# Kernel optimization log

Hardware: AMD Instinct MI355X
Metric: run time of the kernel (lower is better)

The kernel has to match this reference:

```python
import jax, jax.numpy as jnp
import numpy as np

HEADS = 16
DIM_HEAD = 64
QUERY_DIM = 1024
INNER_DIM = HEADS * DIM_HEAD  # 1024
SCALE = DIM_HEAD ** -0.5


def setup_inputs() -> dict:
    key = jax.random.key(0)
    ks = jax.random.split(key, 6)
    B, S = 2, 2048
    hidden_states = jax.random.normal(ks[0], (B, S, QUERY_DIM), dtype=jnp.float32)
    # torch Linear weights are [out, in]; store transposed [in, out] for x @ W
    w_q = jax.random.normal(ks[1], (QUERY_DIM, INNER_DIM), dtype=jnp.float32) * (QUERY_DIM ** -0.5)
    w_k = jax.random.normal(ks[2], (QUERY_DIM, INNER_DIM), dtype=jnp.float32) * (QUERY_DIM ** -0.5)
    w_v = jax.random.normal(ks[3], (QUERY_DIM, INNER_DIM), dtype=jnp.float32) * (QUERY_DIM ** -0.5)
    w_o = jax.random.normal(ks[4], (INNER_DIM, QUERY_DIM), dtype=jnp.float32) * (INNER_DIM ** -0.5)
    b_o = jax.random.normal(ks[5], (QUERY_DIM,), dtype=jnp.float32) * 0.01
    return {"hidden_states": hidden_states, "w_q": w_q, "w_k": w_k, "w_v": w_v, "w_o": w_o, "b_o": b_o}


def reference(hidden_states, w_q, w_k, w_v, w_o, b_o):
    B, S, _ = hidden_states.shape
    # QKV projections (context = hidden_states, i.e. self-attention)
    q = (hidden_states @ w_q).reshape(B, S, HEADS, DIM_HEAD)
    k = (hidden_states @ w_k).reshape(B, S, HEADS, DIM_HEAD)
    v = (hidden_states @ w_v).reshape(B, S, HEADS, DIM_HEAD)
    # scaled dot-product attention; scores materialized as [B, H, S, S]
    scores = jnp.einsum("bqhd,bkhd->bhqk", q, k) * SCALE
    probs = jax.nn.softmax(scores, axis=-1)
    out = jnp.einsum("bhqk,bkhd->bqhd", probs, v).reshape(B, S, INNER_DIM)
    return out @ w_o + b_o
```

## Files before the change

kernel.cpp:

```cpp
#include <hip/hip_runtime.h>
#include <cstdint>
#include <cstddef>

typedef unsigned short u16;
typedef unsigned int u32;
typedef __bf16 bf16x8 __attribute__((ext_vector_type(8)));
typedef float f32x4 __attribute__((ext_vector_type(4)));
typedef float f32x16 __attribute__((ext_vector_type(16)));
typedef u32 u32x2 __attribute__((ext_vector_type(2)));
typedef u32 u32x4 __attribute__((ext_vector_type(4)));

#define AS1 __attribute__((address_space(1)))
#define AS3 __attribute__((address_space(3)))

__device__ __forceinline__ void gld16(const u16* g, u16* l) {
  __builtin_amdgcn_global_load_lds((const AS1 void*)(const void*)g,
                                   (AS3 void*)(void*)l, 16, 0, 0);
}

__device__ __forceinline__ u16 f2bf(float f) {
  union { float f; unsigned u; } x; x.f = f;
  return (u16)((x.u + 0x7fffu + ((x.u >> 16) & 1u)) >> 16);
}

__device__ __forceinline__ float bf2f(u16 u) {
  union { u32 i; float f; } x; x.i = ((u32)u) << 16; return x.f;
}

__device__ __forceinline__ f32x16 zf16() {
  f32x16 v;
#pragma unroll
  for (int i = 0; i < 16; ++i) v[i] = 0.f;
  return v;
}

__global__ void k_cvt(const float* __restrict__ in, u16* __restrict__ out, int n4) {
  int i = blockIdx.x * blockDim.x + threadIdx.x;
  if (i >= n4) return;
  float4 v = reinterpret_cast<const float4*>(in)[i];
  ushort4 o;
  o.x = f2bf(v.x); o.y = f2bf(v.y); o.z = f2bf(v.z); o.w = f2bf(v.w);
  reinterpret_cast<ushort4*>(out)[i] = o;
}

__global__ void k_tr4(const float* __restrict__ wq, const float* __restrict__ wk,
                      const float* __restrict__ wv, const float* __restrict__ wo,
                      u16* __restrict__ Wqkv, u16* __restrict__ Wot) {
  __shared__ float t[32][33];
  const int z = blockIdx.z;
  const float* in = (z == 0) ? wq : (z == 1) ? wk : (z == 2) ? wv : wo;
  u16* out = (z < 3) ? (Wqkv + (size_t)z * 1048576) : Wot;
  int bx = blockIdx.x * 32, by = blockIdx.y * 32;
  int tx = threadIdx.x, ty = threadIdx.y;
#pragma unroll
  for (int j = 0; j < 32; j += 8)
    t[ty + j][tx] = in[(size_t)(by + ty + j) * 1024 + bx + tx];
  __syncthreads();
#pragma unroll
  for (int j = 0; j < 32; j += 8)
    out[(size_t)(bx + ty + j) * 1024 + by + tx] = f2bf(t[tx][ty + j]);
}

__global__ __launch_bounds__(256) void k_gemm_qkv(
    const u16* __restrict__ Xb,
    const u16* __restrict__ Wt,
    u16* __restrict__ Qb,
    u16* __restrict__ Kb,
    u16* __restrict__ Vt) {
  __shared__ __align__(16) u16 As[128][32];
  __shared__ __align__(16) u16 Bs[128][32];
  const int tid = threadIdx.x;
  const int w = tid >> 6, l = tid & 63;
  const int bm = blockIdx.x * 128;
  const int bn = blockIdx.y * 128;
  const int wm = (w >> 1) * 64, wn = (w & 1) * 64;
  const int lm = l & 15, lg = l >> 4;

  f32x4 acc[4][4];
#pragma unroll
  for (int i = 0; i < 4; ++i)
#pragma unroll
    for (int j = 0; j < 4; ++j) acc[i][j] = f32x4{0.f, 0.f, 0.f, 0.f};

  const int srow = w * 16 + (l >> 2);
  const int scol = (l & 3) * 8;
  for (int k0 = 0; k0 < 1024; k0 += 32) {
#pragma unroll
    for (int j = 0; j < 2; ++j) {
      gld16(Xb + (size_t)(bm + j * 64 + srow) * 1024 + k0 + scol, &As[j * 64 + w * 16][0]);
      gld16(Wt + (size_t)(bn + j * 64 + srow) * 1024 + k0 + scol, &Bs[j * 64 + w * 16][0]);
    }
    __syncthreads();
    bf16x8 af[4], bfr[4];
#pragma unroll
    for (int mt = 0; mt < 4; ++mt)
      af[mt] = *reinterpret_cast<const bf16x8*>(&As[wm + mt * 16 + lm][lg * 8]);
#pragma unroll
    for (int nt = 0; nt < 4; ++nt)
      bfr[nt] = *reinterpret_cast<const bf16x8*>(&Bs[wn + nt * 16 + lm][lg * 8]);
#pragma unroll
    for (int mt = 0; mt < 4; ++mt)
#pragma unroll
      for (int nt = 0; nt < 4; ++nt)
        acc[mt][nt] = __builtin_amdgcn_mfma_f32_16x16x32_bf16(af[mt], bfr[nt], acc[mt][nt], 0, 0, 0);
    __syncthreads();
  }
#pragma unroll
  for (int nt = 0; nt < 4; ++nt) {
    int gc = bn + wn + nt * 16 + lm;
    int which = gc >> 10, jc = gc & 1023, h = jc >> 6, d = jc & 63;
#pragma unroll
    for (int mt = 0; mt < 4; ++mt) {
#pragma unroll
      for (int r = 0; r < 4; ++r) {
        int gr = bm + wm + mt * 16 + lg * 4 + r;
        int b = gr >> 11, s = gr & 2047;
        float v = acc[mt][nt][r];
        size_t bh = (size_t)(b * 16 + h);
        if (which == 0)      Qb[(bh * 2048 + s) * 64 + d] = f2bf(v * 0.18033688f);
        else if (which == 1) Kb[(bh * 2048 + s) * 64 + d] = f2bf(v);
        else                 Vt[(bh * 64 + d) * 2048 + s] = f2bf(v);
      }
    }
  }
}

__global__ __launch_bounds__(256) void k_attn(
    const u16* __restrict__ Qb, const u16* __restrict__ Kb,
    const u16* __restrict__ Vt, u16* __restrict__ Opb,
    float* __restrict__ ml) {
  __shared__ __align__(16) u16 Ks[2][64][64];
  __shared__ __align__(16) u16 Vs[2][64][64];
  __shared__ float scb[4][32];
  const int tid = threadIdx.x, w = tid >> 6, l = tid & 63;
  const int lm = l & 31, hi = l >> 5;
  const int kx = lm & 7;
  const int bh = blockIdx.x;
  const int q0 = blockIdx.y * 128 + w * 32;
  const int z = blockIdx.z;
  const int kvbase = z * 1024;
  const u16* Qh = Qb + (size_t)bh * 2048 * 64;
  const u16* Kh = Kb + ((size_t)bh * 2048 + kvbase) * 64;
  const u16* Vh = Vt + (size_t)bh * 64 * 2048 + kvbase;

  bf16x8 qf[4];
#pragma unroll
  for (int c = 0; c < 4; ++c)
    qf[c] = *reinterpret_cast<const bf16x8*>(&Qh[(size_t)(q0 + lm) * 64 + 16 * c + 8 * hi]);

  f32x16 oacc0 = zf16(), oacc1 = zf16();
  float m = -1e30f, lsum = 0.f;

  const int r4 = l >> 2;
  const int vrow = w * 16 + r4;

  {
    u32x2 vreg[2][2];
#pragma unroll
    for (int ch = 0; ch < 2; ++ch) {
      int pg = ((l & 3) + 4 * (r4 & 1) + 4 * ch) & 7;
      int g = pg ^ (r4 & 7);
      int base = ((g >> 1) << 4) | ((g & 1) << 2);
      const u16* src = Vh + (size_t)vrow * 2048 + base;
      vreg[ch][0] = *reinterpret_cast<const u32x2*>(src);
      vreg[ch][1] = *reinterpret_cast<const u32x2*>(src + 8);
    }
#pragma unroll
    for (int j = 0; j < 2; ++j) {
      int row = w * 16 + j * 8 + (l >> 3);
      int g = (l & 7) ^ (row & 7);
      gld16(Kh + (size_t)row * 64 + 8 * g, &Ks[0][w * 16 + j * 8][0]);
    }
#pragma unroll
    for (int ch = 0; ch < 2; ++ch) {
      int pg = ((l & 3) + 4 * (r4 & 1) + 4 * ch) & 7;
      u32x4 pk;
      pk[0] = vreg[ch][0][0]; pk[1] = vreg[ch][0][1];
      pk[2] = vreg[ch][1][0]; pk[3] = vreg[ch][1][1];
      *reinterpret_cast<u32x4*>(&Vs[0][vrow][pg * 8]) = pk;
    }
  }
  __syncthreads();

  for (int t = 0; t < 16; ++t) {
    const int cur = t & 1, nxt = cur ^ 1;
    const int kvn = (t + 1) * 64;
    u32x2 vreg[2][2];
    if (t < 15) {
#pragma unroll
      for (int ch = 0; ch < 2; ++ch) {
        int pg = ((l & 3) + 4 * (r4 & 1) + 4 * ch) & 7;
        int g = pg ^ (r4 & 7);
        int base = ((g >> 1) << 4) | ((g & 1) << 2);
        const u16* src = Vh + (size_t)vrow * 2048 + kvn + base;
        vreg[ch][0] = *reinterpret_cast<const u32x2*>(src);
        vreg[ch][1] = *reinterpret_cast<const u32x2*>(src + 8);
      }
#pragma unroll
      for (int j = 0; j < 2; ++j) {
        int row = w * 16 + j * 8 + (l >> 3);
        int g = (l & 7) ^ (row & 7);
        gld16(Kh + (size_t)(kvn + row) * 64 + 8 * g, &Ks[nxt][w * 16 + j * 8][0]);
      }
    }

    const u16* Kc = &Ks[cur][0][0];
    f32x16 st0 = zf16(), st1 = zf16();
#pragma unroll
    for (int c = 0; c < 4; ++c) {
      bf16x8 kf0 = *reinterpret_cast<const bf16x8*>(Kc + (size_t)lm * 64 + 8 * ((2 * c + hi) ^ kx));
      st0 = __builtin_amdgcn_mfma_f32_32x32x16_bf16(kf0, qf[c], st0, 0, 0, 0);
    }
#pragma unroll
    for (int c = 0; c < 4; ++c) {
      bf16x8 kf1 = *reinterpret_cast<const bf16x8*>(Kc + (size_t)(32 + lm) * 64 + 8 * ((2 * c + hi) ^ kx));
      st1 = __builtin_amdgcn_mfma_f32_32x32x16_bf16(kf1, qf[c], st1, 0, 0, 0);
    }

    float tm = st0[0];
#pragma unroll
    for (int r = 1; r < 16; ++r) tm = fmaxf(tm, st0[r]);
#pragma unroll
    for (int r = 0; r < 16; ++r) tm = fmaxf(tm, st1[r]);
    tm = fmaxf(tm, __shfl_xor(tm, 32));
    if (!__all(tm - m <= 8.0f)) {
      float mnew = fmaxf(m, tm);
      scb[w][lm] = exp2f(m - mnew);
      asm volatile("s_waitcnt lgkmcnt(0)" ::: "memory");
      __builtin_amdgcn_sched_barrier(0);
      lsum *= exp2f(m - mnew);
#pragma unroll
      for (int r = 0; r < 16; ++r) {
        int cr = (r & 3) + 8 * (r >> 2) + 4 * hi;
        float s = scb[w][cr];
        oacc0[r] *= s; oacc1[r] *= s;
      }
      m = mnew;
    }
    float ps = 0.f;
    bf16x8 pf[2][2];
#pragma unroll
    for (int j = 0; j < 2; ++j)
#pragma unroll
      for (int ii = 0; ii < 8; ++ii) {
        float p0 = exp2f(st0[8 * j + ii] - m);
        float p1 = exp2f(st1[8 * j + ii] - m);
        ps += p0 + p1;
        pf[0][j][ii] = (__bf16)p0;
        pf[1][j][ii] = (__bf16)p1;
      }
    ps += __shfl_xor(ps, 32);
    lsum += ps;

    const u16* Vc = &Vs[cur][0][0];
#pragma unroll
    for (int tt = 0; tt < 2; ++tt)
#pragma unroll
      for (int j = 0; j < 2; ++j) {
        int gA = (4 * tt + 2 * j + hi) ^ kx;
        bf16x8 v0 = *reinterpret_cast<const bf16x8*>(Vc + (size_t)lm * 64 + 8 * gA);
        bf16x8 v1 = *reinterpret_cast<const bf16x8*>(Vc + (size_t)(32 + lm) * 64 + 8 * gA);
        oacc0 = __builtin_amdgcn_mfma_f32_32x32x16_bf16(pf[tt][j], v0, oacc0, 0, 0, 0);
        oacc1 = __builtin_amdgcn_mfma_f32_32x32x16_bf16(pf[tt][j], v1, oacc1, 0, 0, 0);
      }

    if (t < 15) {
#pragma unroll
      for (int ch = 0; ch < 2; ++ch) {
        int pg = ((l & 3) + 4 * (r4 & 1) + 4 * ch) & 7;
        u32x4 pk;
        pk[0] = vreg[ch][0][0]; pk[1] = vreg[ch][0][1];
        pk[2] = vreg[ch][1][0]; pk[3] = vreg[ch][1][1];
        *reinterpret_cast<u32x4*>(&Vs[nxt][vrow][pg * 8]) = pk;
      }
    }
    __syncthreads();
  }

  const size_t zb = (size_t)(z * 32 + bh);
  if (!hi) {
    float2 v; v.x = m; v.y = lsum;
    *reinterpret_cast<float2*>(&ml[(zb * 2048 + q0 + lm) * 2]) = v;
  }
  const size_t robase = zb * 2048 + q0;
#pragma unroll
  for (int r = 0; r < 16; ++r) {
    int cr = (r & 3) + 8 * (r >> 2) + 4 * hi;
    size_t ro = (robase + cr) * 64;
    Opb[ro + lm]      = f2bf(oacc0[r]);
    Opb[ro + 32 + lm] = f2bf(oacc1[r]);
  }
}

__global__ __launch_bounds__(256) void k_merge(
    const u16* __restrict__ Opb, const float* __restrict__ ml,
    u16* __restrict__ Ab) {
  int idx = blockIdx.x * 256 + threadIdx.x;
  int d8 = idx & 7, q = (idx >> 3) & 2047, bh = idx >> 14;
  size_t r0 = (size_t)bh * 2048 + q;
  size_t r1 = (size_t)(32 + bh) * 2048 + q;
  float2 ml0 = *reinterpret_cast<const float2*>(&ml[r0 * 2]);
  float2 ml1 = *reinterpret_cast<const float2*>(&ml[r1 * 2]);
  float M = fmaxf(ml0.x, ml1.x);
  float w0 = exp2f(ml0.x - M), w1 = exp2f(ml1.x - M);
  float inv = 1.0f / (w0 * ml0.y + w1 * ml1.y);
  w0 *= inv; w1 *= inv;
  u32x4 a0 = *reinterpret_cast<const u32x4*>(&Opb[r0 * 64 + d8 * 8]);
  u32x4 a1 = *reinterpret_cast<const u32x4*>(&Opb[r1 * 64 + d8 * 8]);
  u32x4 o;
#pragma unroll
  for (int j = 0; j < 4; ++j) {
    float lo = w0 * bf2f((u16)(a0[j] & 0xffff)) + w1 * bf2f((u16)(a1[j] & 0xffff));
    float hb = w0 * bf2f((u16)(a0[j] >> 16))    + w1 * bf2f((u16)(a1[j] >> 16));
    o[j] = (u32)f2bf(lo) | ((u32)f2bf(hb) << 16);
  }
  int b = bh >> 4, h = bh & 15;
  *reinterpret_cast<u32x4*>(&Ab[((size_t)b * 2048 + q) * 1024 + h * 64 + d8 * 8]) = o;
}

__global__ __launch_bounds__(256) void k_gemm_out(
    const u16* __restrict__ Ab,
    const u16* __restrict__ Wot,
    const float* __restrict__ bias, float* __restrict__ out) {
  __shared__ __align__(16) u16 As[128][32];
  __shared__ __align__(16) u16 Bs[128][32];
  const int tid = threadIdx.x;
  const int w = tid >> 6, l = tid & 63;
  const int bm = blockIdx.x * 128;
  const int bn = blockIdx.y * 128;
  const int wm = (w >> 1) * 64, wn = (w & 1) * 64;
  const int lm = l & 15, lg = l >> 4;

  f32x4 acc[4][4];
#pragma unroll
  for (int i = 0; i < 4; ++i)
#pragma unroll
    for (int j = 0; j < 4; ++j) acc[i][j] = f32x4{0.f, 0.f, 0.f, 0.f};

  const int srow = w * 16 + (l >> 2);
  const int scol = (l & 3) * 8;
  for (int k0 = 0; k0 < 1024; k0 += 32) {
#pragma unroll
    for (int j = 0; j < 2; ++j) {
      gld16(Ab  + (size_t)(bm + j * 64 + srow) * 1024 + k0 + scol, &As[j * 64 + w * 16][0]);
      gld16(Wot + (size_t)(bn + j * 64 + srow) * 1024 + k0 + scol, &Bs[j * 64 + w * 16][0]);
    }
    __syncthreads();
    bf16x8 af[4], bfr[4];
#pragma unroll
    for (int mt = 0; mt < 4; ++mt)
      af[mt] = *reinterpret_cast<const bf16x8*>(&As[wm + mt * 16 + lm][lg * 8]);
#pragma unroll
    for (int nt = 0; nt < 4; ++nt)
      bfr[nt] = *reinterpret_cast<const bf16x8*>(&Bs[wn + nt * 16 + lm][lg * 8]);
#pragma unroll
    for (int mt = 0; mt < 4; ++mt)
#pragma unroll
      for (int nt = 0; nt < 4; ++nt)
        acc[mt][nt] = __builtin_amdgcn_mfma_f32_16x16x32_bf16(af[mt], bfr[nt], acc[mt][nt], 0, 0, 0);
    __syncthreads();
  }
#pragma unroll
  for (int nt = 0; nt < 4; ++nt) {
    int gc = bn + wn + nt * 16 + lm;
    float bv = bias[gc];
#pragma unroll
    for (int mt = 0; mt < 4; ++mt) {
#pragma unroll
      for (int r = 0; r < 4; ++r) {
        int gr = bm + wm + mt * 16 + lg * 4 + r;
        out[(size_t)gr * 1024 + gc] = acc[mt][nt][r] + bv;
      }
    }
  }
}

extern "C" void kernel_launch(void* const* d_in, const int* in_sizes, int n_in,
                              void* d_out, int out_size, void* d_ws, size_t ws_size,
                              hipStream_t stream) {
  const float* X  = (const float*)d_in[0];
  const float* wq = (const float*)d_in[1];
  const float* wk = (const float*)d_in[2];
  const float* wv = (const float*)d_in[3];
  const float* wo = (const float*)d_in[4];
  const float* bo = (const float*)d_in[5];
  float* out = (float*)d_out;

  char* ws = (char*)d_ws;
  u16*   Xb   = (u16*)(ws);
  u16*   Wqkv = (u16*)(ws + (size_t)(8u  << 20));
  u16*   Wot  = (u16*)(ws + (size_t)(14u << 20));
  u16*   Qb   = (u16*)(ws + (size_t)(16u << 20));
  u16*   Kb   = (u16*)(ws + (size_t)(24u << 20));
  u16*   Vt   = (u16*)(ws + (size_t)(32u << 20));
  u16*   Opb  = (u16*)(ws + (size_t)(40u << 20));
  float* ml   = (float*)(ws + (size_t)(8u << 20));
  u16*   Ab   = (u16*)(ws);

  k_cvt<<<4096, 256, 0, stream>>>(X, Xb, 4096 * 1024 / 4);
  k_tr4<<<dim3(32, 32, 4), dim3(32, 8), 0, stream>>>(wq, wk, wv, wo, Wqkv, Wot);
  k_gemm_qkv<<<dim3(32, 24), 256, 0, stream>>>(Xb, Wqkv, Qb, Kb, Vt);
  k_attn<<<dim3(32, 16, 2), 256, 0, stream>>>(Qb, Kb, Vt, Opb, ml);
  k_merge<<<2048, 256, 0, stream>>>(Opb, ml, Ab);
  k_gemm_out<<<dim3(32, 8), 256, 0, stream>>>(Ab, Wot, bo, out);
}
```

Before: 147.6 us.

## Load V fragments directly from global into registers, bypassing shared memory

```diff
diff --git a/kernel.cpp b/kernel.cpp
--- a/kernel.cpp
+++ b/kernel.cpp
@@ -32,6 +32,12 @@
 #pragma unroll
   for (int i = 0; i < 16; ++i) v[i] = 0.f;
   return v;
+}
+
+__device__ __forceinline__ bf16x8 mk8(u32x2 a, u32x2 b) {
+  union { u32x4 u; bf16x8 v; } x;
+  x.u[0] = a[0]; x.u[1] = a[1]; x.u[2] = b[0]; x.u[3] = b[1];
+  return x.v;
 }
 
 __global__ void k_cvt(const float* __restrict__ in, u16* __restrict__ out, int n4) {
@@ -130,7 +136,6 @@
     const u16* __restrict__ Vt, u16* __restrict__ Opb,
     float* __restrict__ ml) {
   __shared__ __align__(16) u16 Ks[2][64][64];
-  __shared__ __align__(16) u16 Vs[2][64][64];
   __shared__ float scb[4][32];
   const int tid = threadIdx.x, w = tid >> 6, l = tid & 63;
   const int lm = l & 31, hi = l >> 5;
@@ -138,10 +143,9 @@
   const int bh = blockIdx.x;
   const int q0 = blockIdx.y * 128 + w * 32;
   const int z = blockIdx.z;
-  const int kvbase = z * 1024;
   const u16* Qh = Qb + (size_t)bh * 2048 * 64;
-  const u16* Kh = Kb + ((size_t)bh * 2048 + kvbase) * 64;
-  const u16* Vh = Vt + (size_t)bh * 64 * 2048 + kvbase;
+  const u16* Kh = Kb + ((size_t)bh * 2048 + z * 1024) * 64;
+  const u16* Vh = Vt + (size_t)bh * 64 * 2048 + z * 1024;
 
   bf16x8 qf[4];
 #pragma unroll
@@ -151,51 +155,33 @@
   f32x16 oacc0 = zf16(), oacc1 = zf16();
   float m = -1e30f, lsum = 0.f;
 
-  const int r4 = l >> 2;
-  const int vrow = w * 16 + r4;
-
-  {
-    u32x2 vreg[2][2];
-#pragma unroll
-    for (int ch = 0; ch < 2; ++ch) {
-      int pg = ((l & 3) + 4 * (r4 & 1) + 4 * ch) & 7;
-      int g = pg ^ (r4 & 7);
-      int base = ((g >> 1) << 4) | ((g & 1) << 2);
-      const u16* src = Vh + (size_t)vrow * 2048 + base;
-      vreg[ch][0] = *reinterpret_cast<const u32x2*>(src);
-      vreg[ch][1] = *reinterpret_cast<const u32x2*>(src + 8);
-    }
-#pragma unroll
-    for (int j = 0; j < 2; ++j) {
-      int row = w * 16 + j * 8 + (l >> 3);
-      int g = (l & 7) ^ (row & 7);
-      gld16(Kh + (size_t)row * 64 + 8 * g, &Ks[0][w * 16 + j * 8][0]);
-    }
-#pragma unroll
-    for (int ch = 0; ch < 2; ++ch) {
-      int pg = ((l & 3) + 4 * (r4 & 1) + 4 * ch) & 7;
-      u32x4 pk;
-      pk[0] = vreg[ch][0][0]; pk[1] = vreg[ch][0][1];
-      pk[2] = vreg[ch][1][0]; pk[3] = vreg[ch][1][1];
-      *reinterpret_cast<u32x4*>(&Vs[0][vrow][pg * 8]) = pk;
-    }
+  const char* vp0 = (const char*)(Vh + (size_t)lm * 2048 + 4 * hi);
+  const char* vp1 = (const char*)(Vh + (size_t)(32 + lm) * 2048 + 4 * hi);
+
+#pragma unroll
+  for (int j = 0; j < 2; ++j) {
+    int row = w * 16 + j * 8 + (l >> 3);
+    int g = (l & 7) ^ (row & 7);
+    gld16(Kh + (size_t)row * 64 + 8 * g, &Ks[0][w * 16 + j * 8][0]);
   }
   __syncthreads();
 
   for (int t = 0; t < 16; ++t) {
     const int cur = t & 1, nxt = cur ^ 1;
-    const int kvn = (t + 1) * 64;
-    u32x2 vreg[2][2];
+
+    u32x2 va[2][2][2], vb[2][2][2];
+#pragma unroll
+    for (int tt = 0; tt < 2; ++tt)
+#pragma unroll
+      for (int j = 0; j < 2; ++j) {
+        va[tt][j][0] = *reinterpret_cast<const u32x2*>(vp0 + 64 * tt + 32 * j);
+        va[tt][j][1] = *reinterpret_cast<const u32x2*>(vp0 + 64 * tt + 32 * j + 16);
+        vb[tt][j][0] = *reinterpret_cast<const u32x2*>(vp1 + 64 * tt + 32 * j);
+        vb[tt][j][1] = *reinterpret_cast<const u32x2*>(vp1 + 64 * tt + 32 * j + 16);
+      }
+
     if (t < 15) {
-#pragma unroll
-      for (int ch = 0; ch < 2; ++ch) {
-        int pg = ((l & 3) + 4 * (r4 & 1) + 4 * ch) & 7;
-        int g = pg ^ (r4 & 7);
-        int base = ((g >> 1) << 4) | ((g & 1) << 2);
-        const u16* src = Vh + (size_t)vrow * 2048 + kvn + base;
-        vreg[ch][0] = *reinterpret_cast<const u32x2*>(src);
-        vreg[ch][1] = *reinterpret_cast<const u32x2*>(src + 8);
-      }
+      const int kvn = (t + 1) * 64;
 #pragma unroll
       for (int j = 0; j < 2; ++j) {
         int row = w * 16 + j * 8 + (l >> 3);
@@ -206,6 +192,7 @@
 
     const u16* Kc = &Ks[cur][0][0];
     f32x16 st0 = zf16(), st1 = zf16();
+    __builtin_amdgcn_s_setprio(1);
 #pragma unroll
     for (int c = 0; c < 4; ++c) {
       bf16x8 kf0 = *reinterpret_cast<const bf16x8*>(Kc + (size_t)lm * 64 + 8 * ((2 * c + hi) ^ kx));
@@ -216,13 +203,16 @@
       bf16x8 kf1 = *reinterpret_cast<const bf16x8*>(Kc + (size_t)(32 + lm) * 64 + 8 * ((2 * c + hi) ^ kx));
       st1 = __builtin_amdgcn_mfma_f32_32x32x16_bf16(kf1, qf[c], st1, 0, 0, 0);
     }
-
-    float tm = st0[0];
-#pragma unroll
-    for (int r = 1; r < 16; ++r) tm = fmaxf(tm, st0[r]);
-#pragma unroll
-    for (int r = 0; r < 16; ++r) tm = fmaxf(tm, st1[r]);
-    tm = fmaxf(tm, __shfl_xor(tm, 32));
+    __builtin_amdgcn_s_setprio(0);
+
+    float mx[16];
+#pragma unroll
+    for (int r = 0; r < 16; ++r) mx[r] = fmaxf(st0[r], st1[r]);
+#pragma unroll
+    for (int s = 8; s; s >>= 1)
+#pragma unroll
+      for (int r = 0; r < s; ++r) mx[r] = fmaxf(mx[r], mx[r + s]);
+    float tm = fmaxf(mx[0], __shfl_xor(mx[0], 32));
     if (!__all(tm - m <= 8.0f)) {
       float mnew = fmaxf(m, tm);
       scb[w][lm] = exp2f(m - mnew);
@@ -252,28 +242,19 @@
     ps += __shfl_xor(ps, 32);
     lsum += ps;
 
-    const u16* Vc = &Vs[cur][0][0];
+    __builtin_amdgcn_s_setprio(1);
 #pragma unroll
     for (int tt = 0; tt < 2; ++tt)
 #pragma unroll
       for (int j = 0; j < 2; ++j) {
-        int gA = (4 * tt + 2 * j + hi) ^ kx;
-        bf16x8 v0 = *reinterpret_cast<const bf16x8*>(Vc + (size_t)lm * 64 + 8 * gA);
-        bf16x8 v1 = *reinterpret_cast<const bf16x8*>(Vc + (size_t)(32 + lm) * 64 + 8 * gA);
+        bf16x8 v0 = mk8(va[tt][j][0], va[tt][j][1]);
+        bf16x8 v1 = mk8(vb[tt][j][0], vb[tt][j][1]);
         oacc0 = __builtin_amdgcn_mfma_f32_32x32x16_bf16(pf[tt][j], v0, oacc0, 0, 0, 0);
         oacc1 = __builtin_amdgcn_mfma_f32_32x32x16_bf16(pf[tt][j], v1, oacc1, 0, 0, 0);
       }
-
-    if (t < 15) {
-#pragma unroll
-      for (int ch = 0; ch < 2; ++ch) {
-        int pg = ((l & 3) + 4 * (r4 & 1) + 4 * ch) & 7;
-        u32x4 pk;
-        pk[0] = vreg[ch][0][0]; pk[1] = vreg[ch][0][1];
-        pk[2] = vreg[ch][1][0]; pk[3] = vreg[ch][1][1];
-        *reinterpret_cast<u32x4*>(&Vs[nxt][vrow][pg * 8]) = pk;
-      }
-    }
+    __builtin_amdgcn_s_setprio(0);
+
+    vp0 += 128; vp1 += 128;
     __syncthreads();
   }
 
```

Result: slower. 203.9 us (+38.2%).
